# Kernel tuning notes

Hardware: AMD Instinct MI355X
Metric: run time of the kernel (lower is better)

The kernel has to match this reference:

```python
import jax, jax.numpy as jnp
import numpy as np
import math

H = 1024          # hidden_size
NH = 16           # num heads
HD = H // NH      # head_dim = 64
ORDER = 2         # torsion_order
RANK = 64         # torsion_rank


def setup_inputs() -> dict:
    key = jax.random.key(0)
    ks = jax.random.split(key, 16)
    B, S = 2, 2048
    std = 0.02
    inp = {
        "hidden_states": jax.random.normal(ks[0], (B, S, H), jnp.float32),
        # projection weights stored [in, out] (equivalent to torch Linear W^T)
        "Wq": jax.random.normal(ks[1], (H, H), jnp.float32) * std,
        "bq": jnp.zeros((H,), jnp.float32),
        "Wk": jax.random.normal(ks[2], (H, H), jnp.float32) * std,
        "bk": jnp.zeros((H,), jnp.float32),
        "Wv": jax.random.normal(ks[3], (H, H), jnp.float32) * std,
        "bv": jnp.zeros((H,), jnp.float32),
        "Wo": jax.random.normal(ks[4], (H, H), jnp.float32) * std,
        "bo": jnp.zeros((H,), jnp.float32),
        "q_torsion_a": jax.random.normal(ks[5], (ORDER, H, RANK), jnp.float32) * 0.01,
        "q_torsion_b": jax.random.normal(ks[6], (ORDER, RANK, H), jnp.float32) * 0.01,
        "k_torsion_a": jax.random.normal(ks[7], (ORDER, H, RANK), jnp.float32) * 0.01,
        "k_torsion_b": jax.random.normal(ks[8], (ORDER, RANK, H), jnp.float32) * 0.01,
        "torsion_coupling": jnp.asarray(0.1, jnp.float32),
    }
    return inp


def _apply_torsion(x, ta, tb, coupling):
    # x: [B,S,H]; ta: [ORDER,H,R]; tb: [ORDER,R,H]
    corr = jnp.zeros_like(x)
    for n in range(ORDER):
        low = jnp.einsum('bsh,hr->bsr', x, ta[n])
        lin = jnp.einsum('bsr,rh->bsh', low, tb[n])
        phase = (2.0 * math.pi * (n + 1)) * lin
        corr = corr + jnp.sin(phase) * lin / (n + 1)
    return x + jax.nn.sigmoid(coupling) * corr


def reference(hidden_states, Wq, bq, Wk, bk, Wv, bv, Wo, bo,
              q_torsion_a, q_torsion_b, k_torsion_a, k_torsion_b,
              torsion_coupling):
    B, S, _ = hidden_states.shape
    q = hidden_states @ Wq + bq
    k = hidden_states @ Wk + bk
    v = hidden_states @ Wv + bv
    q = _apply_torsion(q, q_torsion_a, q_torsion_b, torsion_coupling)
    k = _apply_torsion(k, k_torsion_a, k_torsion_b, torsion_coupling)
    # [B, NH, S, HD]
    q = q.reshape(B, S, NH, HD).transpose(0, 2, 1, 3)
    k = k.reshape(B, S, NH, HD).transpose(0, 2, 1, 3)
    v = v.reshape(B, S, NH, HD).transpose(0, 2, 1, 3)
    scale = HD ** -0.5
    attn = jnp.einsum('bhqd,bhkd->bhqk', q, k) * scale
    attn = jax.nn.softmax(attn, axis=-1)
    out = jnp.einsum('bhqk,bhkd->bhqd', attn, v)
    out = out.transpose(0, 2, 1, 3).reshape(B, S, H)
    return out @ Wo + bo
```

## Files before the change

kernel.cpp:

```cpp
#include <hip/hip_runtime.h>
#include <hip/hip_bf16.h>
#include <cstdint>
#include <cstddef>

typedef __bf16 bf16_t;
typedef __bf16 bf16x8 __attribute__((ext_vector_type(8)));
typedef float f32x4 __attribute__((ext_vector_type(4)));

static __device__ __forceinline__ void st_out(float* p, float v) { *p = v; }
static __device__ __forceinline__ void st_out(bf16_t* p, float v) { *p = (bf16_t)v; }

static __device__ __forceinline__ void async_cp16(const bf16_t* g, bf16_t* l) {
  __builtin_amdgcn_global_load_lds(
      (const __attribute__((address_space(1))) void*)g,
      (__attribute__((address_space(3))) void*)l, 16, 0, 0);
}

__global__ __launch_bounds__(256) void prep(const float* __restrict__ hs, bf16_t* __restrict__ hsb,
                                            const float* __restrict__ Wq, const float* __restrict__ Wk,
                                            const float* __restrict__ Wv, const float* __restrict__ Wo,
                                            bf16_t* __restrict__ BtExt, bf16_t* __restrict__ WoT,
                                            bf16_t* __restrict__ Wqb, bf16_t* __restrict__ Wkb,
                                            const float* __restrict__ qta, const float* __restrict__ kta,
                                            bf16_t* __restrict__ qtaT, bf16_t* __restrict__ ktaT,
                                            const float* __restrict__ qtb, const float* __restrict__ ktb,
                                            bf16_t* __restrict__ qtbT, bf16_t* __restrict__ ktbT,
                                            const float* __restrict__ bq, const float* __restrict__ bk,
                                            const float* __restrict__ bv, float* __restrict__ biasN) {
  __shared__ float tile[32][33];
  const int bid = blockIdx.x, t = threadIdx.x;
  const int tx = t & 31, ty = t >> 5;

  if (bid < 2048) {
    int i = (bid * 256 + t) * 8;
    float4 a = *(const float4*)(hs + i);
    float4 b = *(const float4*)(hs + i + 4);
    union { bf16_t h[8]; uint4 u; } p;
    p.h[0] = (bf16_t)a.x; p.h[1] = (bf16_t)a.y; p.h[2] = (bf16_t)a.z; p.h[3] = (bf16_t)a.w;
    p.h[4] = (bf16_t)b.x; p.h[5] = (bf16_t)b.y; p.h[6] = (bf16_t)b.z; p.h[7] = (bf16_t)b.w;
    *(uint4*)(hsb + i) = p.u;
  } else if (bid < 6144) {
    int r = bid - 2048, z = r >> 10, r10 = r & 1023;
    int bx = (r10 & 31) * 32, by = (r10 >> 5) * 32;
    const float* src = z == 0 ? Wq : z == 1 ? Wk : z == 2 ? Wv : Wo;
    bf16_t* dst = z == 3 ? WoT : BtExt + (size_t)z * 1048576;
    bf16_t* sd = z == 0 ? Wqb : z == 1 ? Wkb : nullptr;
#pragma unroll
    for (int i = 0; i < 4; ++i) {
      float v = src[(size_t)(by + ty + i * 8) * 1024 + bx + tx];
      tile[ty + i * 8][tx] = v;
      if (sd) sd[(size_t)(by + ty + i * 8) * 1024 + bx + tx] = (bf16_t)v;
    }
    __syncthreads();
#pragma unroll
    for (int i = 0; i < 4; ++i)
      dst[(size_t)(bx + ty + i * 8) * 1024 + by + tx] = (bf16_t)tile[tx][ty + i * 8];
  } else if (bid < 6400) {
    int r = bid - 6144, z = r >> 6, r6 = r & 63;
    int bx = (r6 & 1) * 32, by = (r6 >> 1) * 32;
    const float* src = ((z >> 1) ? kta : qta) + (size_t)(z & 1) * 65536;
    bf16_t* dst = ((z >> 1) ? ktaT : qtaT) + (size_t)(z & 1) * 65536;
#pragma unroll
    for (int i = 0; i < 4; ++i)
      tile[ty + i * 8][tx] = src[(size_t)(by + ty + i * 8) * 64 + bx + tx];
    __syncthreads();
#pragma unroll
    for (int i = 0; i < 4; ++i)
      dst[(size_t)(bx + ty + i * 8) * 1024 + by + tx] = (bf16_t)tile[tx][ty + i * 8];
  } else if (bid < 6656) {
    int r = bid - 6400, z = r >> 6, r6 = r & 63;
    int bx = (r6 & 31) * 32, by = (r6 >> 5) * 32;
    const float* src = ((z >> 1) ? ktb : qtb) + (size_t)(z & 1) * 65536;
    bf16_t* dst = ((z >> 1) ? ktbT : qtbT) + (size_t)(z & 1) * 65536;
#pragma unroll
    for (int i = 0; i < 4; ++i)
      tile[ty + i * 8][tx] = src[(size_t)(by + ty + i * 8) * 1024 + bx + tx];
    __syncthreads();
#pragma unroll
    for (int i = 0; i < 4; ++i)
      dst[(size_t)(bx + ty + i * 8) * 64 + by + tx] = (bf16_t)tile[tx][ty + i * 8];
  } else if (bid < 6668) {
    int i = (bid - 6656) * 256 + t;
    biasN[i] = (i < 1024) ? bq[i] : (i < 2048 ? bk[i - 1024] : bv[i - 2048]);
  } else {
    int j = t;
    const float* b = (j < 128) ? bq : bk;
    const float* ta = ((j < 128) ? qta : kta) + (size_t)((j >> 6) & 1) * 65536;
    int rr = j & 63;
    float s = 0.f;
    for (int h = 0; h < 1024; ++h) s += b[h] * ta[(size_t)h * 64 + rr];
    biasN[3072 + j] = s;
  }
}

template <typename OutT>
static __device__ __forceinline__ void gemm_core_async(const bf16_t* __restrict__ A, int lda,
                                                       const bf16_t* __restrict__ Bt, int ldb,
                                                       OutT* __restrict__ C, int ldc,
                                                       const float* __restrict__ bias, int K,
                                                       int bx, int by) {
  __shared__ bf16_t As[128][32];
  __shared__ bf16_t Bs[128][32];
  const int m0 = by * 128, n0 = bx * 128;
  const int t = threadIdx.x, w = t >> 6, lane = t & 63;
  const int wm = (w >> 1) * 64, wn = (w & 1) * 64;
  const int quad = lane >> 4, l16 = lane & 15;
  const int sra = lane >> 2, sca = (lane & 3) * 8;
  const bf16_t* Ag0 = A + (size_t)(m0 + w * 16 + sra) * lda + sca;
  const bf16_t* Ag1 = A + (size_t)(m0 + 64 + w * 16 + sra) * lda + sca;
  const bf16_t* Bg0 = Bt + (size_t)(n0 + w * 16 + sra) * ldb + sca;
  const bf16_t* Bg1 = Bt + (size_t)(n0 + 64 + w * 16 + sra) * ldb + sca;
  bf16_t* la0 = &As[0][0] + w * 512;
  bf16_t* la1 = &As[0][0] + 2048 + w * 512;
  bf16_t* lb0 = &Bs[0][0] + w * 512;
  bf16_t* lb1 = &Bs[0][0] + 2048 + w * 512;

  f32x4 acc[4][4] = {};
  for (int k0 = 0; k0 < K; k0 += 32) {
    __syncthreads();
    async_cp16(Ag0 + k0, la0);
    async_cp16(Ag1 + k0, la1);
    async_cp16(Bg0 + k0, lb0);
    async_cp16(Bg1 + k0, lb1);
    __syncthreads();
    bf16x8 af[4], bfr[4];
#pragma unroll
    for (int i = 0; i < 4; ++i)
      af[i] = *(const bf16x8*)&As[wm + i * 16 + l16][quad * 8];
#pragma unroll
    for (int j = 0; j < 4; ++j)
      bfr[j] = *(const bf16x8*)&Bs[wn + j * 16 + l16][quad * 8];
#pragma unroll
    for (int i = 0; i < 4; ++i)
#pragma unroll
      for (int j = 0; j < 4; ++j)
        acc[i][j] = __builtin_amdgcn_mfma_f32_16x16x32_bf16(af[i], bfr[j], acc[i][j], 0, 0, 0);
  }
#pragma unroll
  for (int i = 0; i < 4; ++i) {
    int row = m0 + wm + i * 16 + quad * 4;
#pragma unroll
    for (int j = 0; j < 4; ++j) {
      int col = n0 + wn + j * 16 + l16;
      float bv = bias ? bias[col] : 0.f;
#pragma unroll
      for (int r = 0; r < 4; ++r)
        st_out(&C[(size_t)(row + r) * ldc + col], acc[i][j][r] + bv);
    }
  }
}

template <typename OutT>
static __device__ __forceinline__ void gemm_core_async64(const bf16_t* __restrict__ A, int lda,
                                                         const bf16_t* __restrict__ Bt, int ldb,
                                                         OutT* __restrict__ C, int ldc,
                                                         const float* __restrict__ bias, int K,
                                                         int bx, int by) {
  __shared__ bf16_t As[64][32];
  __shared__ bf16_t Bs[128][32];
  const int m0 = by * 64, n0 = bx * 128;
  const int t = threadIdx.x, w = t >> 6, lane = t & 63;
  const int wm = (w >> 1) * 32, wn = (w & 1) * 64;
  const int quad = lane >> 4, l16 = lane & 15;
  const int sra = lane >> 2, sca = (lane & 3) * 8;
  const bf16_t* Ag0 = A + (size_t)(m0 + w * 16 + sra) * lda + sca;
  const bf16_t* Bg0 = Bt + (size_t)(n0 + w * 16 + sra) * ldb + sca;
  const bf16_t* Bg1 = Bt + (size_t)(n0 + 64 + w * 16 + sra) * ldb + sca;
  bf16_t* la0 = &As[0][0] + w * 512;
  bf16_t* lb0 = &Bs[0][0] + w * 512;
  bf16_t* lb1 = &Bs[0][0] + 2048 + w * 512;

  f32x4 acc[2][4] = {};
  for (int k0 = 0; k0 < K; k0 += 32) {
    __syncthreads();
    async_cp16(Ag0 + k0, la0);
    async_cp16(Bg0 + k0, lb0);
    async_cp16(Bg1 + k0, lb1);
    __syncthreads();
    bf16x8 af[2], bfr[4];
#pragma unroll
    for (int i = 0; i < 2; ++i)
      af[i] = *(const bf16x8*)&As[wm + i * 16 + l16][quad * 8];
#pragma unroll
    for (int j = 0; j < 4; ++j)
      bfr[j] = *(const bf16x8*)&Bs[wn + j * 16 + l16][quad * 8];
#pragma unroll
    for (int i = 0; i < 2; ++i)
#pragma unroll
      for (int j = 0; j < 4; ++j)
        acc[i][j] = __builtin_amdgcn_mfma_f32_16x16x32_bf16(af[i], bfr[j], acc[i][j], 0, 0, 0);
  }
#pragma unroll
  for (int i = 0; i < 2; ++i) {
    int row = m0 + wm + i * 16 + quad * 4;
#pragma unroll
    for (int j = 0; j < 4; ++j) {
      int col = n0 + wn + j * 16 + l16;
      float bv = bias ? bias[col] : 0.f;
#pragma unroll
      for (int r = 0; r < 4; ++r)
        st_out(&C[(size_t)(row + r) * ldc + col], acc[i][j][r] + bv);
    }
  }
}

__global__ __launch_bounds__(256) void gemm_qkv(const bf16_t* __restrict__ A,
                                                const bf16_t* __restrict__ Bt,
                                                bf16_t* __restrict__ C,
                                                const float* __restrict__ biasN) {
  gemm_core_async<bf16_t>(A, 1024, Bt, 1024, C, 3328, biasN, 1024, blockIdx.x, blockIdx.y);
}

__global__ __launch_bounds__(256) void gemm_out(const bf16_t* __restrict__ A,
                                                const bf16_t* __restrict__ Bt,
                                                float* __restrict__ C,
                                                const float* __restrict__ bo) {
  gemm_core_async64<float>(A, 1024, Bt, 1024, C, 1024, bo, 1024, blockIdx.x, blockIdx.y);
}

__global__ __launch_bounds__(256) void gemm_wta(const bf16_t* __restrict__ qtaT,
                                                const bf16_t* __restrict__ ktaT,
                                                const bf16_t* __restrict__ Wqb,
                                                const bf16_t* __restrict__ Wkb,
                                                bf16_t* __restrict__ BtExt) {
  int z = blockIdx.z;
  gemm_core_async64<bf16_t>(z ? ktaT : qtaT, 1024, z ? Wkb : Wqb, 1024,
                            BtExt + (size_t)(3072 + z * 128) * 1024, 1024,
                            nullptr, 1024, blockIdx.x, blockIdx.y);
}

__global__ __launch_bounds__(256) void lin_torsion_fused(const bf16_t* __restrict__ qtbT,
                                                         const bf16_t* __restrict__ ktbT,
                                                         bf16_t* __restrict__ qkv,
                                                         const float* __restrict__ coupling) {
  __shared__ bf16_t As[128][136];
  __shared__ bf16_t Bs0[128][72];
  __shared__ bf16_t Bs1[128][72];
  const int z = blockIdx.z;
  const bf16_t* Low = qkv + 3072 + z * 128;
  const bf16_t* Tb = z ? ktbT : qtbT;
  bf16_t* X = qkv + z * 1024;

  const int m0 = blockIdx.y * 128, n0 = blockIdx.x * 128;
  const int t = threadIdx.x, w = t >> 6, lane = t & 63;
  const int wm = (w >> 1) * 64, wn = (w & 1) * 64;
  const int quad = lane >> 4, l16 = lane & 15;

  {
    const int sr = t >> 1, sc = (t & 1) * 64;
    const bf16_t* Ag = Low + (size_t)(m0 + sr) * 3328 + sc;
#pragma unroll
    for (int i = 0; i < 8; ++i)
      *(float4*)&As[sr][sc + 8 * i] = *(const float4*)(Ag + 8 * i);
    const int br = t >> 1, bc = (t & 1) * 32;
    const bf16_t* Bg0 = Tb + (size_t)(n0 + br) * 64 + bc;
    const bf16_t* Bg1 = Bg0 + 65536;
#pragma unroll
    for (int i = 0; i < 4; ++i) {
      *(float4*)&Bs0[br][bc + 8 * i] = *(const float4*)(Bg0 + 8 * i);
      *(float4*)&Bs1[br][bc + 8 * i] = *(const float4*)(Bg1 + 8 * i);
    }
  }
  __syncthreads();

  f32x4 acc0[4][4] = {}, acc1[4][4] = {};
#pragma unroll
  for (int ks = 0; ks < 2; ++ks) {
    bf16x8 a0[4], a1[4];
#pragma unroll
    for (int i = 0; i < 4; ++i) {
      a0[i] = *(const bf16x8*)&As[wm + i * 16 + l16][ks * 32 + quad * 8];
      a1[i] = *(const bf16x8*)&As[wm + i * 16 + l16][64 + ks * 32 + quad * 8];
    }
#pragma unroll
    for (int j = 0; j < 4; ++j) {
      bf16x8 b0 = *(const bf16x8*)&Bs0[wn + j * 16 + l16][ks * 32 + quad * 8];
      bf16x8 b1 = *(const bf16x8*)&Bs1[wn + j * 16 + l16][ks * 32 + quad * 8];
#pragma unroll
      for (int i = 0; i < 4; ++i) {
        acc0[i][j] = __builtin_amdgcn_mfma_f32_16x16x32_bf16(a0[i], b0, acc0[i][j], 0, 0, 0);
        acc1[i][j] = __builtin_amdgcn_mfma_f32_16x16x32_bf16(a1[i], b1, acc1[i][j], 0, 0, 0);
      }
    }
  }

  const float PI2 = 6.283185307179586f;
  const float sig = 1.f / (1.f + __expf(-coupling[0]));
  const float scale = z ? 1.f : 0.1803368801111204f;
#pragma unroll
  for (int i = 0; i < 4; ++i) {
#pragma unroll
    for (int j = 0; j < 4; ++j) {
#pragma unroll
      for (int r = 0; r < 4; ++r) {
        int row = m0 + wm + i * 16 + quad * 4 + r;
        int col = n0 + wn + j * 16 + l16;
        size_t idx = (size_t)row * 3328 + col;
        float l1 = acc0[i][j][r], l2 = acc1[i][j][r];
        float corr = __sinf(PI2 * l1) * l1 + __sinf(2.f * PI2 * l2) * l2 * 0.5f;
        X[idx] = (bf16_t)(((float)X[idx] + sig * corr) * scale);
      }
    }
  }
}

__global__ __launch_bounds__(256, 2) void flash_attn(const bf16_t* __restrict__ qkv,
                                                     bf16_t* __restrict__ aout) {
  constexpr int LD = 3328, SEQ = 2048;
  const int qb = blockIdx.x, bh = blockIdx.y;
  const int b = bh >> 4, h = bh & 15;
  const size_t base = (size_t)b * SEQ * LD + h * 64;
  const bf16_t* Qg = qkv + base;
  const bf16_t* Kg = qkv + base + 1024;
  const bf16_t* Vg = qkv + base + 2048;

  __shared__ __align__(16) unsigned char smem[34816];
  bf16_t(*VT0)[136] = (bf16_t(*)[136])smem;
  bf16_t(*VT1)[136] = (bf16_t(*)[136])(smem + 17408);
  float* LDSo = (float*)smem;
  float* Lred = (float*)(smem + 24576);
  float* invL = (float*)(smem + 28672);

  const int t = threadIdx.x, w = t >> 6, lane = t & 63;
  const int kw = w >> 1, qw = w & 1;
  const int quad = lane >> 4, l16 = lane & 15;
  const int q0 = qb * 128;

  bf16x8 qf[4][2];
  {
    const bf16_t* Qrow = Qg + (size_t)(q0 + qw * 64 + l16) * LD + quad * 8;
#pragma unroll
    for (int nf = 0; nf < 4; ++nf)
#pragma unroll
      for (int ks = 0; ks < 2; ++ks)
        qf[nf][ks] = *(const bf16x8*)(Qrow + (size_t)(nf * 16) * LD + ks * 32);
  }

  f32x4 o[4][4] = {};
  float l_part[4] = {0.f, 0.f, 0.f, 0.f};

  const int vg = t >> 3, vcb = (t & 7) * 8;
  const int colb = (((vg >> 3) << 5) | ((vg & 3) << 3) | (((vg >> 2) & 1) << 2)) ^ ((t & 7) << 3);
  const bf16_t* Vbase = Vg + (size_t)(vg * 4) * LD + vcb;
  const bf16_t* Krow = Kg + (size_t)(kw * 64 + l16) * LD + quad * 8;

  float4 vr[4];

#pragma unroll
  for (int kk = 0; kk < 4; ++kk)
    vr[kk] = *(const float4*)(Vbase + (size_t)kk * LD);
#pragma unroll
  for (int cc = 0; cc < 8; ++cc) {
    union { bf16_t h[4]; uint2 u; } pk;
#pragma unroll
    for (int kk = 0; kk < 4; ++kk) pk.h[kk] = ((const bf16_t*)&vr[kk])[cc];
    *(uint2*)&VT0[vcb + cc][colb] = pk.u;
  }
#pragma unroll
  for (int kk = 0; kk < 4; ++kk)
    vr[kk] = *(const float4*)(Vbase + (size_t)(128 + kk) * LD);
  __syncthreads();

  for (int k0 = 0; k0 < SEQ; k0 += 128) {
    bf16_t(*VTc)[136] = ((k0 >> 7) & 1) ? VT1 : VT0;
    bf16_t(*VTn)[136] = ((k0 >> 7) & 1) ? VT0 : VT1;

    bf16x8 kf[4][2];
#pragma unroll
    for (int jk = 0; jk < 4; ++jk)
#pragma unroll
      for (int ks = 0; ks < 2; ++ks)
        kf[jk][ks] = *(const bf16x8*)(Krow + (size_t)(k0 + jk * 16) * LD + ks * 32);

    f32x4 st[4][4] = {};
    __builtin_amdgcn_s_setprio(1);
#pragma unroll
    for (int ks = 0; ks < 2; ++ks)
#pragma unroll
      for (int jk = 0; jk < 4; ++jk)
#pragma unroll
        for (int nf = 0; nf < 4; ++nf)
          st[jk][nf] = __builtin_amdgcn_mfma_f32_16x16x32_bf16(kf[jk][ks], qf[nf][ks], st[jk][nf], 0, 0, 0);
    __builtin_amdgcn_s_setprio(0);

    bf16x8 Pp[2][4];
#pragma unroll
    for (int g = 0; g < 2; ++g)
#pragma unroll
      for (int nf = 0; nf < 4; ++nf) {
        union { bf16_t hh[8]; bf16x8 v; } ph;
#pragma unroll
        for (int b2 = 0; b2 < 2; ++b2)
#pragma unroll
          for (int r = 0; r < 4; ++r) {
            float p = exp2f(st[g * 2 + b2][nf][r]);
            l_part[nf] += p;
            ph.hh[b2 * 4 + r] = (bf16_t)p;
          }
        Pp[g][nf] = ph.v;
      }

    if (k0 + 128 < SEQ) {
#pragma unroll
      for (int cc = 0; cc < 8; ++cc) {
        union { bf16_t h[4]; uint2 u; } pk;
#pragma unroll
        for (int kk = 0; kk < 4; ++kk) pk.h[kk] = ((const bf16_t*)&vr[kk])[cc];
        *(uint2*)&VTn[vcb + cc][colb] = pk.u;
      }
      if (k0 + 256 < SEQ) {
#pragma unroll
        for (int kk = 0; kk < 4; ++kk)
          vr[kk] = *(const float4*)(Vbase + (size_t)(k0 + 256 + kk) * LD);
      }
    }

#pragma unroll
    for (int g = 0; g < 2; ++g) {
      bf16x8 vf[4];
#pragma unroll
      for (int jd = 0; jd < 4; ++jd) {
        int row = jd * 16 + l16;
        int col = (kw * 64 + g * 32 + quad * 8) ^ ((((row >> 3) & 7)) << 3);
        vf[jd] = *(const bf16x8*)&VTc[row][col];
      }
      __builtin_amdgcn_s_setprio(1);
#pragma unroll
      for (int jd = 0; jd < 4; ++jd)
#pragma unroll
        for (int nf = 0; nf < 4; ++nf)
          o[jd][nf] = __builtin_amdgcn_mfma_f32_16x16x32_bf16(vf[jd], Pp[g][nf], o[jd][nf], 0, 0, 0);
      __builtin_amdgcn_s_setprio(0);
    }

    __syncthreads();
  }

#pragma unroll
  for (int nf = 0; nf < 4; ++nf)
    Lred[((kw * 2 + qw) * 4 + quad) * 64 + nf * 16 + l16] = l_part[nf];
  __syncthreads();
  if (t < 128) {
    int qw2 = t >> 6, ql = t & 63;
    float s = 0.f;
#pragma unroll
    for (int kw2 = 0; kw2 < 2; ++kw2)
#pragma unroll
      for (int qd = 0; qd < 4; ++qd)
        s += Lred[((kw2 * 2 + qw2) * 4 + qd) * 64 + ql];
    invL[t] = 1.f / s;
  }
  __syncthreads();

  const int rq = t >> 1, rc0 = (t & 1) * 8;
#pragma unroll
  for (int jd = 0; jd < 4; ++jd) {
#pragma unroll
    for (int nf = 0; nf < 4; ++nf)
      *(f32x4*)&LDSo[(size_t)(kw * 128 + qw * 64 + nf * 16 + l16) * 24 + quad * 4] = o[jd][nf];
    __syncthreads();
    f32x4 a0 = *(const f32x4*)&LDSo[(size_t)rq * 24 + rc0];
    f32x4 a1 = *(const f32x4*)&LDSo[(size_t)(128 + rq) * 24 + rc0];
    f32x4 b0 = *(const f32x4*)&LDSo[(size_t)rq * 24 + rc0 + 4];
    f32x4 b1 = *(const f32x4*)&LDSo[(size_t)(128 + rq) * 24 + rc0 + 4];
    float iv = invL[rq];
    union { bf16_t h[8]; uint4 u; } pk;
#pragma unroll
    for (int r = 0; r < 4; ++r) {
      pk.h[r] = (bf16_t)((a0[r] + a1[r]) * iv);
      pk.h[4 + r] = (bf16_t)((b0[r] + b1[r]) * iv);
    }
    *(uint4*)&aout[(size_t)(b * SEQ + q0 + rq) * 1024 + h * 64 + jd * 16 + rc0] = pk.u;
    if (jd < 3) __syncthreads();
  }
}

extern "C" void kernel_launch(void* const* d_in, const int* in_sizes, int n_in,
                              void* d_out, int out_size, void* d_ws, size_t ws_size,
                              hipStream_t stream) {
  const float* hs   = (const float*)d_in[0];
  const float* Wq   = (const float*)d_in[1];
  const float* bq   = (const float*)d_in[2];
  const float* Wk   = (const float*)d_in[3];
  const float* bk   = (const float*)d_in[4];
  const float* Wv   = (const float*)d_in[5];
  const float* bv   = (const float*)d_in[6];
  const float* Wo   = (const float*)d_in[7];
  const float* bo   = (const float*)d_in[8];
  const float* qta  = (const float*)d_in[9];
  const float* qtb  = (const float*)d_in[10];
  const float* kta  = (const float*)d_in[11];
  const float* ktb  = (const float*)d_in[12];
  const float* coup = (const float*)d_in[13];
  float* out = (float*)d_out;

  uint8_t* ws = (uint8_t*)d_ws;
  bf16_t* hsb   = (bf16_t*)(ws);
  bf16_t* aout  = (bf16_t*)(ws);
  bf16_t* BtExt = (bf16_t*)(ws + 8388608);
  bf16_t* WoT   = (bf16_t*)(ws + 16777216);
  float*  biasN = (float*)(ws + 18874368);
  bf16_t* qkv   = (bf16_t*)(ws + 18890752);
  bf16_t* Wqb   = (bf16_t*)(ws + 46153728);
  bf16_t* Wkb   = (bf16_t*)(ws + 48250880);
  bf16_t* qtaT  = (bf16_t*)(ws + 50348032);
  bf16_t* ktaT  = (bf16_t*)(ws + 50610176);
  bf16_t* qtbT  = (bf16_t*)(ws + 50872320);
  bf16_t* ktbT  = (bf16_t*)(ws + 51134464);

  dim3 b256(256);

  prep<<<6669, b256, 0, stream>>>(hs, hsb, Wq, Wk, Wv, Wo, BtExt, WoT, Wqb, Wkb,
                                  qta, kta, qtaT, ktaT, qtb, ktb, qtbT, ktbT,
                                  bq, bk, bv, biasN);
  gemm_wta<<<dim3(8, 2, 2), b256, 0, stream>>>(qtaT, ktaT, Wqb, Wkb, BtExt);
  gemm_qkv<<<dim3(26, 32), b256, 0, stream>>>(hsb, BtExt, qkv, biasN);
  lin_torsion_fused<<<dim3(8, 32, 2), b256, 0, stream>>>(qtbT, ktbT, qkv, coup);
  flash_attn<<<dim3(16, 32), b256, 0, stream>>>(qkv, aout);
  gemm_out<<<dim3(8, 64), b256, 0, stream>>>(aout, WoT, out, bo);
}
```

Baseline: 290.9 us.

## Stage K tiles through double-buffered async LDS and swizzle GEMM block order

In flash attention, K tiles are now copied asynchronously into a swizzled, double-buffered LDS area with global_load_lds, and the next tile is prefetched while the current one is used. Before, each wave read its K fragments directly from global memory. This should cut redundant global traffic and hide load latency, at the cost of roughly doubling LDS per block while still fitting two blocks per CU. The QKV and output GEMMs also remap block IDs into groups so that neighbouring blocks share operand tiles in L2.

Result: faster. 283.3 us (-2.6%).

```diff
diff --git a/kernel.cpp b/kernel.cpp
--- a/kernel.cpp
+++ b/kernel.cpp
@@ -208,14 +208,18 @@
                                                 const bf16_t* __restrict__ Bt,
                                                 bf16_t* __restrict__ C,
                                                 const float* __restrict__ biasN) {
-  gemm_core_async<bf16_t>(A, 1024, Bt, 1024, C, 3328, biasN, 1024, blockIdx.x, blockIdx.y);
+  int id = blockIdx.y * 26 + blockIdx.x;
+  int nid = (id & 7) * 104 + (id >> 3);
+  gemm_core_async<bf16_t>(A, 1024, Bt, 1024, C, 3328, biasN, 1024, nid % 26, nid / 26);
 }
 
 __global__ __launch_bounds__(256) void gemm_out(const bf16_t* __restrict__ A,
                                                 const bf16_t* __restrict__ Bt,
                                                 float* __restrict__ C,
                                                 const float* __restrict__ bo) {
-  gemm_core_async64<float>(A, 1024, Bt, 1024, C, 1024, bo, 1024, blockIdx.x, blockIdx.y);
+  int id = blockIdx.y * 8 + blockIdx.x;
+  int nid = (id & 7) * 64 + (id >> 3);
+  gemm_core_async64<float>(A, 1024, Bt, 1024, C, 1024, bo, 1024, nid & 7, nid >> 3);
 }
 
 __global__ __launch_bounds__(256) void gemm_wta(const bf16_t* __restrict__ qtaT,
@@ -314,9 +318,11 @@
   const bf16_t* Kg = qkv + base + 1024;
   const bf16_t* Vg = qkv + base + 2048;
 
-  __shared__ __align__(16) unsigned char smem[34816];
+  __shared__ __align__(16) unsigned char smem[67584];
   bf16_t(*VT0)[136] = (bf16_t(*)[136])smem;
   bf16_t(*VT1)[136] = (bf16_t(*)[136])(smem + 17408);
+  bf16_t* Kl0 = (bf16_t*)(smem + 34816);
+  bf16_t* Kl1 = (bf16_t*)(smem + 51200);
   float* LDSo = (float*)smem;
   float* Lred = (float*)(smem + 24576);
   float* invL = (float*)(smem + 28672);
@@ -342,10 +348,17 @@
   const int vg = t >> 3, vcb = (t & 7) * 8;
   const int colb = (((vg >> 3) << 5) | ((vg & 3) << 3) | (((vg >> 2) & 1) << 2)) ^ ((t & 7) << 3);
   const bf16_t* Vbase = Vg + (size_t)(vg * 4) * LD + vcb;
-  const bf16_t* Krow = Kg + (size_t)(kw * 64 + l16) * LD + quad * 8;
+
+  const bf16_t* Kstg = Kg + (size_t)(w * 8 + (lane >> 3)) * LD + ((lane & 7) ^ (lane >> 3)) * 8;
 
   float4 vr[4];
 
+  {
+    bf16_t* dst = Kl0 + w * 512;
+#pragma unroll
+    for (int c = 0; c < 4; ++c)
+      async_cp16(Kstg + (size_t)(c * 32) * LD, dst + c * 2048);
+  }
 #pragma unroll
   for (int kk = 0; kk < 4; ++kk)
     vr[kk] = *(const float4*)(Vbase + (size_t)kk * LD);
@@ -362,15 +375,28 @@
   __syncthreads();
 
   for (int k0 = 0; k0 < SEQ; k0 += 128) {
-    bf16_t(*VTc)[136] = ((k0 >> 7) & 1) ? VT1 : VT0;
-    bf16_t(*VTn)[136] = ((k0 >> 7) & 1) ? VT0 : VT1;
+    const int cur = (k0 >> 7) & 1;
+    bf16_t(*VTc)[136] = cur ? VT1 : VT0;
+    bf16_t(*VTn)[136] = cur ? VT0 : VT1;
+    const bf16_t* Kc = cur ? Kl1 : Kl0;
+
+    if (k0 + 128 < SEQ) {
+      bf16_t* dst = (cur ? Kl0 : Kl1) + w * 512;
+#pragma unroll
+      for (int c = 0; c < 4; ++c)
+        async_cp16(Kstg + (size_t)(k0 + 128 + c * 32) * LD, dst + c * 2048);
+    }
 
     bf16x8 kf[4][2];
 #pragma unroll
-    for (int jk = 0; jk < 4; ++jk)
-#pragma unroll
-      for (int ks = 0; ks < 2; ++ks)
-        kf[jk][ks] = *(const bf16x8*)(Krow + (size_t)(k0 + jk * 16) * LD + ks * 32);
+    for (int jk = 0; jk < 4; ++jk) {
+      int row = kw * 64 + jk * 16 + l16;
+#pragma unroll
+      for (int ks = 0; ks < 2; ++ks) {
+        int ch = (ks * 4 + quad) ^ (l16 & 7);
+        kf[jk][ks] = *(const bf16x8*)&Kc[row * 64 + ch * 8];
+      }
+    }
 
     f32x4 st[4][4] = {};
     __builtin_amdgcn_s_setprio(1);
```
